# Performance work log

Measured on AMD Instinct MI355X. Metric: run time of the kernel, lower is better.

Reference implementation:

```python
import jax, jax.numpy as jnp
import numpy as np

DIM = 1024
HEADS = 16
HEAD_DIM = DIM // HEADS
SCALE = HEAD_DIM ** -0.5
EPS = 1e-5


def _ln(x, g, b):
    m = jnp.mean(x, axis=-1, keepdims=True)
    v = jnp.mean((x - m) ** 2, axis=-1, keepdims=True)
    return (x - m) * jax.lax.rsqrt(v + EPS) * g + b


def setup_inputs() -> dict:
    key = jax.random.key(0)
    ks = jax.random.split(key, 12)
    B, N, C = 4, 1024, DIM
    s = lambda fan: 1.0 / np.sqrt(fan)
    return {
        "src_q": jax.random.normal(ks[0], (B, N, C), jnp.float32),
        "src_kv": jax.random.normal(ks[1], (B, N, C), jnp.float32),
        "gq": jnp.ones((C,), jnp.float32), "bq": jnp.zeros((C,), jnp.float32),
        "gkv": jnp.ones((C,), jnp.float32), "bkv": jnp.zeros((C,), jnp.float32),
        "Wq": jax.random.normal(ks[2], (C, C), jnp.float32) * s(C),
        "Wkv": jax.random.normal(ks[3], (C, 2 * C), jnp.float32) * s(C),
        "Wproj": jax.random.normal(ks[4], (C, C), jnp.float32) * s(C),
        "bproj": jnp.zeros((C,), jnp.float32),
        "gn": jnp.ones((C,), jnp.float32), "bn": jnp.zeros((C,), jnp.float32),
        "W1": jax.random.normal(ks[5], (C, 4 * C), jnp.float32) * s(C),
        "b1": jnp.zeros((4 * C,), jnp.float32),
        "W2": jax.random.normal(ks[6], (4 * C, C), jnp.float32) * s(4 * C),
        "b2": jnp.zeros((C,), jnp.float32),
    }


def reference(src_q, src_kv, gq, bq, gkv, bkv, Wq, Wkv, Wproj, bproj,
              gn, bn, W1, b1, W2, b2):
    B, N, C = src_q.shape
    qn = _ln(src_q, gq, bq)
    kvn = _ln(src_kv, gkv, bkv)
    # Q: [B, H, N, d]
    Q = (qn @ Wq).reshape(B, N, HEADS, HEAD_DIM).transpose(0, 2, 1, 3)
    KV = (kvn @ Wkv).reshape(B, N, 2, HEADS, HEAD_DIM).transpose(2, 0, 3, 1, 4)
    K, V = KV[0], KV[1]
    attn = jnp.einsum('bhqd,bhkd->bhqk', Q, K) * SCALE
    attn = jax.nn.softmax(attn, axis=-1)
    # NOTE: original code multiplies by scale a second time here (faithful)
    x = jnp.einsum('bhqk,bhkd->bhqd', attn, V) * SCALE
    x = x.transpose(0, 2, 1, 3).reshape(B, N, C)
    x = x @ Wproj + bproj
    src = src_q + x               # residual (drop_path = identity in eval)
    src = _ln(src, gn, bn)
    h = jax.nn.gelu(src @ W1 + b1, approximate=False)
    src2 = h @ W2 + b2
    return src + src2
```

## Files before the change

### kernel.cpp

```cpp
#include <hip/hip_runtime.h>
#include <hip/hip_bf16.h>
#include <math.h>

typedef __bf16 bf16;
typedef __bf16 bf16x2 __attribute__((ext_vector_type(2)));
typedef __bf16 bf16x8 __attribute__((ext_vector_type(8)));
typedef float f32x4 __attribute__((ext_vector_type(4)));
typedef float f32x16 __attribute__((ext_vector_type(16)));
typedef unsigned int u32;
typedef unsigned int u32x2 __attribute__((ext_vector_type(2)));
typedef unsigned int u32x4 __attribute__((ext_vector_type(4)));

#define SCALE 0.125f

#define GLOAD_LDS16(gptr, lptr)                                      \
  __builtin_amdgcn_global_load_lds(                                  \
      (const __attribute__((address_space(1))) void*)(gptr),         \
      (__attribute__((address_space(3))) void*)(lptr), 16, 0, 0)

template <int N>
__device__ __forceinline__ void vmcnt_wait() {
  if constexpr (N == 0) asm volatile("s_waitcnt vmcnt(0)" ::: "memory");
  else if constexpr (N == 4) asm volatile("s_waitcnt vmcnt(4)" ::: "memory");
  else if constexpr (N == 6) asm volatile("s_waitcnt vmcnt(6)" ::: "memory");
  else static_assert(N == 0 || N == 4 || N == 6, "unsupported vmcnt");
}

__device__ __forceinline__ void xcd_swz(int gx, int gy, int& x, int& y) {
  int w = blockIdx.x + gx * blockIdx.y;
  int nwg = gx * gy;
  int wp = (w & 7) * (nwg >> 3) + (w >> 3);
  int xi = wp & 7;
  int t = wp >> 3;
  y = t % gy;
  x = (t / gy) * 8 + xi;
}

__device__ __forceinline__ u32 pk_bf16(float lo, float hi) {
  bf16x2 t;
  t[0] = (bf16)lo;
  t[1] = (bf16)hi;
  return __builtin_bit_cast(u32, t);
}

__device__ __forceinline__ void plane32_swap(u32& a, u32& b) {
  asm volatile("v_permlane32_swap_b32 %0, %1" : "+v"(a), "+v"(b));
}

__global__ __launch_bounds__(256) void ln_f32(const float* __restrict__ x,
                                              const float* __restrict__ g,
                                              const float* __restrict__ b,
                                              bf16* __restrict__ y) {
  long base = (long)blockIdx.x * 1024;
  int tid = threadIdx.x;
  float v[4];
#pragma unroll
  for (int i = 0; i < 4; i++) v[i] = x[base + tid + i * 256];
  float s1 = v[0] + v[1] + v[2] + v[3];
  float s2 = v[0] * v[0] + v[1] * v[1] + v[2] * v[2] + v[3] * v[3];
#pragma unroll
  for (int off = 32; off; off >>= 1) {
    s1 += __shfl_xor(s1, off);
    s2 += __shfl_xor(s2, off);
  }
  __shared__ float aux[2][4];
  int wave = tid >> 6, lane = tid & 63;
  if (lane == 0) { aux[0][wave] = s1; aux[1][wave] = s2; }
  __syncthreads();
  float S1 = aux[0][0] + aux[0][1] + aux[0][2] + aux[0][3];
  float S2 = aux[1][0] + aux[1][1] + aux[1][2] + aux[1][3];
  float mean = S1 * (1.0f / 1024.0f);
  float var = S2 * (1.0f / 1024.0f) - mean * mean;
  float rs = rsqrtf(var + 1e-5f);
#pragma unroll
  for (int i = 0; i < 4; i++) {
    int c = tid + i * 256;
    y[base + c] = (bf16)(((v[i] - mean) * rs) * g[c] + b[c]);
  }
}

__global__ __launch_bounds__(256) void transpose_w(const float* __restrict__ W,
                                                   bf16* __restrict__ Wt,
                                                   int K, int N) {
  __shared__ bf16 tile[64][66];
  int n0 = blockIdx.x * 64, k0 = blockIdx.y * 64;
  int c = threadIdx.x & 63, r4 = threadIdx.x >> 6;
#pragma unroll
  for (int i = 0; i < 16; i++)
    tile[i * 4 + r4][c] = (bf16)W[(long)(k0 + i * 4 + r4) * N + n0 + c];
  __syncthreads();
#pragma unroll
  for (int i = 0; i < 16; i++)
    Wt[(long)(n0 + i * 4 + r4) * K + k0 + c] = tile[c][i * 4 + r4];
}

__global__ __launch_bounds__(256) void extract_vt(const bf16* __restrict__ KV,
                                                  bf16* __restrict__ Vt) {
  __shared__ bf16 tile[64][66];
  int bh = blockIdx.z, b = bh >> 4, h = bh & 15;
  const bf16* src = KV + (long)b * 1024 * 2048 + 1024 + h * 64;
  bf16* dst = Vt + (long)bh * 64 * 1024;
  int n0 = blockIdx.x * 64;
  int c = threadIdx.x & 63, r4 = threadIdx.x >> 6;
#pragma unroll
  for (int i = 0; i < 16; i++)
    tile[i * 4 + r4][c] = src[(long)(n0 + i * 4 + r4) * 2048 + c];
  __syncthreads();
#pragma unroll
  for (int i = 0; i < 16; i++)
    dst[(long)(i * 4 + r4) * 1024 + n0 + c] = tile[c][i * 4 + r4];
}

__global__ __launch_bounds__(256) void attn_fused(
    const bf16* __restrict__ Q,
    const bf16* __restrict__ KV,
    const bf16* __restrict__ Vt,
    bf16* __restrict__ X) {
  __shared__ __align__(16) bf16 Qs[128 * 64];
  __shared__ __align__(16) bf16 Ks[2][64 * 128];
  __shared__ __align__(16) bf16 Vs[2][64 * 128];
  int tid = threadIdx.x, wave = tid >> 6, lane = tid & 63;
  int l31 = lane & 31, h = lane >> 5;
  int bqx, bhy;
  xcd_swz(8, 64, bqx, bhy);
  int bh = bhy, b = bh >> 4, hd = bh & 15;
  const bf16* Qb = Q + (long)b * 1048576 + hd * 64;
  const bf16* Kb = KV + (long)b * 2097152 + hd * 64;
  const bf16* Vb = Vt + (long)bh * 65536;
  bf16* Xb = X + (long)b * 1048576 + hd * 64;
  int q0 = bqx * 128;

  const bf16* gk[4];
  const bf16* gv[4];
  int eoKV[4];
#pragma unroll
  for (int t = 0; t < 4; t++) {
    int eo = (t * 256 + tid) * 8;
    eoKV[t] = eo;
    int r2 = eo >> 7, pp = (eo & 127) >> 3, q = pp ^ (r2 & 15);
    gk[t] = &Kb[(long)(r2 + ((q >> 3) << 6)) * 2048 + ((q & 7) << 3)];
    gv[t] = &Vb[(long)r2 * 1024 + (q << 3)];
  }

#pragma unroll
  for (int t = 0; t < 4; t++) {
    int eo = (t * 256 + tid) * 8;
    int r = eo >> 6, p = (eo & 63) >> 3;
    int c = (p ^ (r & 7)) << 3;
    GLOAD_LDS16(&Qb[(long)(q0 + r) * 1024 + c], &Qs[eo]);
  }
#pragma unroll
  for (int t = 0; t < 4; t++) GLOAD_LDS16(gk[t], &Ks[0][eoKV[t]]);
#pragma unroll
  for (int t = 0; t < 4; t++) GLOAD_LDS16(gv[t], &Vs[0][eoKV[t]]);
  __syncthreads();

  bf16x8 qf[4];
  {
    int r = wave * 32 + l31;
#pragma unroll
    for (int dw = 0; dw < 4; dw++) {
      int p = (dw * 2 + h) ^ (r & 7);
      qf[dw] = *(const bf16x8*)&Qs[r * 64 + p * 8];
    }
  }

  const float C = 0.18033688011112042f;
  float m_run = -1e30f, l_run = 0.0f;
  f32x16 acc[2] = {};
  int cur = 0;

  for (int kc = 0; kc < 8; kc++) {
    if (kc < 7) {
#pragma unroll
      for (int t = 0; t < 4; t++)
        GLOAD_LDS16(gk[t] + (long)(kc + 1) * 128 * 2048, &Ks[cur ^ 1][eoKV[t]]);
#pragma unroll
      for (int t = 0; t < 4; t++)
        GLOAD_LDS16(gv[t] + (kc + 1) * 128, &Vs[cur ^ 1][eoKV[t]]);
    }
    const bf16* ks = Ks[cur];
    const bf16* vs = Vs[cur];

    f32x16 s[4] = {};
#pragma unroll
    for (int kt = 0; kt < 4; kt++) {
      int k = kt * 32 + l31;
      int r2 = k & 63, hi = k >> 6;
#pragma unroll
      for (int dw = 0; dw < 4; dw++) {
        int p = (hi * 8 + dw * 2 + h) ^ (r2 & 15);
        bf16x8 kf = *(const bf16x8*)&ks[r2 * 128 + p * 8];
        s[kt] = __builtin_amdgcn_mfma_f32_32x32x16_bf16(kf, qf[dw], s[kt], 0, 0, 0);
      }
    }

    float mk[4];
#pragma unroll
    for (int kt = 0; kt < 4; kt++) {
      float m01 = fmaxf(fmaxf(s[kt][0], s[kt][1]), fmaxf(s[kt][2], s[kt][3]));
      float m23 = fmaxf(fmaxf(s[kt][4], s[kt][5]), fmaxf(s[kt][6], s[kt][7]));
      float m45 = fmaxf(fmaxf(s[kt][8], s[kt][9]), fmaxf(s[kt][10], s[kt][11]));
      float m67 = fmaxf(fmaxf(s[kt][12], s[kt][13]), fmaxf(s[kt][14], s[kt][15]));
      mk[kt] = fmaxf(fmaxf(m01, m23), fmaxf(m45, m67));
    }
    float mx = fmaxf(fmaxf(mk[0], mk[1]), fmaxf(mk[2], mk[3]));
    mx = fmaxf(mx, __shfl_xor(mx, 32));
    float m_new = fmaxf(m_run, mx);
    float alpha = exp2f((m_run - m_new) * C);
    m_run = m_new;
    float mc = m_new * C;
    float rk[4];
#pragma unroll
    for (int kt = 0; kt < 4; kt++) {
      float r0 = 0.0f;
#pragma unroll
      for (int r = 0; r < 16; r++) {
        float pv = exp2f(s[kt][r] * C - mc);
        s[kt][r] = pv;
        r0 += pv;
      }
      rk[kt] = r0;
    }
    float rs = (rk[0] + rk[1]) + (rk[2] + rk[3]);
    rs += __shfl_xor(rs, 32);
    l_run = l_run * alpha + rs;
#pragma unroll
    for (int nt = 0; nt < 2; nt++)
#pragma unroll
      for (int r = 0; r < 16; r++) acc[nt][r] *= alpha;

#pragma unroll
    for (int kw = 0; kw < 8; kw++) {
      int kt = kw >> 1, rb = (kw & 1) * 8;
      u32 wA = pk_bf16(s[kt][rb + 0], s[kt][rb + 1]);
      u32 wB = pk_bf16(s[kt][rb + 2], s[kt][rb + 3]);
      u32 wC = pk_bf16(s[kt][rb + 4], s[kt][rb + 5]);
      u32 wD = pk_bf16(s[kt][rb + 6], s[kt][rb + 7]);
      plane32_swap(wA, wC);
      plane32_swap(wB, wD);
      u32x4 wv = {wA, wB, wC, wD};
      bf16x8 pf = __builtin_bit_cast(bf16x8, wv);
#pragma unroll
      for (int nt = 0; nt < 2; nt++) {
        int r2 = nt * 32 + l31;
        int p = (kw * 2 + h) ^ (r2 & 15);
        bf16x8 vf = *(const bf16x8*)&vs[r2 * 128 + p * 8];
        acc[nt] = __builtin_amdgcn_mfma_f32_32x32x16_bf16(vf, pf, acc[nt], 0, 0, 0);
      }
    }

    if (kc < 7) {
      __syncthreads();
      cur ^= 1;
    }
  }

  float fs = SCALE / l_run;
  bf16* Os = Qs;
  int qrow = wave * 32 + l31;
#pragma unroll
  for (int nt = 0; nt < 2; nt++)
#pragma unroll
    for (int g = 0; g < 4; g++) {
      u32 w0 = pk_bf16(acc[nt][g * 4 + 0] * fs, acc[nt][g * 4 + 1] * fs);
      u32 w1 = pk_bf16(acc[nt][g * 4 + 2] * fs, acc[nt][g * 4 + 3] * fs);
      int s8 = nt * 8 + g * 2 + h;
      int phys = s8 ^ (qrow & 15);
      u32x2 wv = {w0, w1};
      *(u32x2*)&Os[qrow * 64 + phys * 4] = wv;
    }
  int rrow = wave * 32 + (lane >> 1);
  int cbase = (lane & 1) * 32;
#pragma unroll
  for (int t2 = 0; t2 < 4; t2++) {
    int s0 = (lane & 1) * 8 + t2 * 2;
    u32x2 a = *(u32x2*)&Os[rrow * 64 + ((s0 ^ (rrow & 15)) * 4)];
    u32x2 bb = *(u32x2*)&Os[rrow * 64 + (((s0 + 1) ^ (rrow & 15)) * 4)];
    u32x4 o4 = {a[0], a[1], bb[0], bb[1]};
    *(u32x4*)&Xb[(long)(q0 + rrow) * 1024 + cbase + t2 * 8] = o4;
  }
}

template <int BM, int BN, int WR, int WC, int EPI, int CF32, int RBF16>
__global__ __launch_bounds__(512) void gemm_p(
    const bf16* __restrict__ A, int lda,
    const bf16* __restrict__ B, int ldb,
    void* __restrict__ Cv, int ldc, int K,
    const float* __restrict__ bias,
    const void* __restrict__ resv, int ldr) {
  constexpr int MT = BM / (16 * WR);
  constexpr int NT = BN / (16 * WC);
  constexpr int L = (BM + BN) / 64;
  constexpr int LA = BM / 64;
  constexpr int AE = BM * 64;
  constexpr int BUFE = (BM + BN) * 64;
  __shared__ __align__(16) bf16 lds[3 * BUFE];
  int tid = threadIdx.x;
  int wave = tid >> 6, lane = tid & 63;
  int wm = wave / WC, wn = wave % WC;
  int quad = lane >> 4, l16 = lane & 15;
  int bx, by;
  xcd_swz(gridDim.x, gridDim.y, bx, by);
  int m0 = by * BM, n0 = bx * BN;

  const bf16* gp[L];
  int lo[L];
#pragma unroll
  for (int i = 0; i < L; i++) {
    if (i < LA) {
      int eo = (i * 512 + tid) * 8;
      int r = eo >> 6, p = (eo & 63) >> 3;
      int c = (p ^ (r & 7)) << 3;
      gp[i] = &A[(long)(m0 + r) * lda + c];
      lo[i] = eo;
    } else {
      int eo = ((i - LA) * 512 + tid) * 8;
      int r = eo >> 6, p = (eo & 63) >> 3;
      int c = (p ^ (r & 7)) << 3;
      gp[i] = &B[(long)(n0 + r) * ldb + c];
      lo[i] = AE + eo;
    }
  }

  int ntk = K >> 6;
#pragma unroll
  for (int i = 0; i < L; i++) GLOAD_LDS16(gp[i], &lds[lo[i]]);
#pragma unroll
  for (int i = 0; i < L; i++) gp[i] += 64;
#pragma unroll
  for (int i = 0; i < L; i++) GLOAD_LDS16(gp[i], &lds[BUFE + lo[i]]);
#pragma unroll
  for (int i = 0; i < L; i++) gp[i] += 64;
  vmcnt_wait<L>();
  asm volatile("" ::: "memory");
  __builtin_amdgcn_s_barrier();

  f32x4 acc[MT][NT] = {};
  int b = 0;
  for (int t = 0; t < ntk; t++) {
    const bf16* Al = &lds[b * BUFE];
    const bf16* Bl = &lds[b * BUFE + AE];
    int b2 = b + 2; if (b2 >= 3) b2 -= 3;
    bool more = (t + 2) < ntk;

    bf16x8 af[2][MT], bv[2][NT];
#pragma unroll
    for (int ks = 0; ks < 2; ks++) {
#pragma unroll
      for (int mt = 0; mt < MT; mt++) {
        int row = wm * (BM / WR) + mt * 16 + l16;
        int p = (ks * 4 + quad) ^ (row & 7);
        af[ks][mt] = *(const bf16x8*)&Al[row * 64 + p * 8];
      }
#pragma unroll
      for (int nt = 0; nt < NT; nt++) {
        int row = wn * (BN / WC) + nt * 16 + l16;
        int p = (ks * 4 + quad) ^ (row & 7);
        bv[ks][nt] = *(const bf16x8*)&Bl[row * 64 + p * 8];
      }
    }
    if (more) {
#pragma unroll
      for (int i = 0; i < L; i++) GLOAD_LDS16(gp[i], &lds[b2 * BUFE + lo[i]]);
    }
    asm volatile("s_waitcnt lgkmcnt(0)" ::: "memory");
    __builtin_amdgcn_sched_barrier(0);
    __builtin_amdgcn_s_setprio(1);
#pragma unroll
    for (int ks = 0; ks < 2; ks++)
#pragma unroll
      for (int mt = 0; mt < MT; mt++)
#pragma unroll
        for (int nt = 0; nt < NT; nt++)
          acc[mt][nt] = __builtin_amdgcn_mfma_f32_16x16x32_bf16(
              af[ks][mt], bv[ks][nt], acc[mt][nt], 0, 0, 0);
    __builtin_amdgcn_s_setprio(0);
    __builtin_amdgcn_sched_barrier(0);
    if (more) {
      vmcnt_wait<L>();
    } else if (t + 1 < ntk) {
      vmcnt_wait<0>();
    }
    if (t + 1 < ntk) {
      asm volatile("" ::: "memory");
      __builtin_amdgcn_s_barrier();
    }
#pragma unroll
    for (int i = 0; i < L; i++) gp[i] += 64;
    b += 1; if (b == 3) b = 0;
  }

  int gm = m0 + wm * (BM / WR), gn = n0 + wn * (BN / WC);
#pragma unroll
  for (int nt = 0; nt < NT; nt++) {
    int col = gn + nt * 16 + l16;
    float bvb = (EPI != 0) ? bias[col] : 0.0f;
#pragma unroll
    for (int mt = 0; mt < MT; mt++) {
#pragma unroll
      for (int r = 0; r < 4; r++) {
        int row = gm + mt * 16 + quad * 4 + r;
        float v = acc[mt][nt][r] + bvb;
        if (EPI == 2) {
          v = 0.5f * v * (1.0f + erff(v * 0.70710678118654752f));
        } else if (EPI == 1) {
          float rv = RBF16 ? (float)((const bf16*)resv)[(long)row * ldr + col]
                           : ((const float*)resv)[(long)row * ldr + col];
          v += rv;
        }
        if (CF32)
          ((float*)Cv)[(long)row * ldc + col] = v;
        else
          ((bf16*)Cv)[(long)row * ldc + col] = (bf16)v;
      }
    }
  }
}

template <int EPI, int CF32, int RBF16>
__global__ __launch_bounds__(512) void gemm_256(
    const bf16* __restrict__ A, int lda,
    const bf16* __restrict__ B, int ldb,
    void* __restrict__ Cv, int ldc, int K,
    const float* __restrict__ bias,
    const void* __restrict__ resv, int ldr) {
  constexpr int AE = 256 * 64;
  constexpr int BUFE = 512 * 64;
  __shared__ __align__(16) bf16 lds[2 * BUFE];
  int tid = threadIdx.x;
  int wave = tid >> 6, lane = tid & 63;
  int wm = wave >> 2, wn = wave & 3;
  int quad = lane >> 4, l16 = lane & 15;
  int bx, by;
  xcd_swz(gridDim.x, gridDim.y, bx, by);
  int m0 = by * 256, n0 = bx * 256;

  const bf16* gp[8];
  int lo[8];
#pragma unroll
  for (int i = 0; i < 8; i++) {
    if (i < 4) {
      int eo = (i * 512 + tid) * 8;
      int r = eo >> 6, p = (eo & 63) >> 3;
      int c = (p ^ (r & 7)) << 3;
      gp[i] = &A[(long)(m0 + r) * lda + c];
      lo[i] = eo;
    } else {
      int eo = ((i - 4) * 512 + tid) * 8;
      int r = eo >> 6, p = (eo & 63) >> 3;
      int c = (p ^ (r & 7)) << 3;
      gp[i] = &B[(long)(n0 + r) * ldb + c];
      lo[i] = AE + eo;
    }
  }

  int ntk = K >> 6;
#pragma unroll
  for (int i = 0; i < 8; i++) GLOAD_LDS16(gp[i], &lds[lo[i]]);
#pragma unroll
  for (int i = 0; i < 8; i++) gp[i] += 64;
  vmcnt_wait<0>();
  asm volatile("" ::: "memory");
  __builtin_amdgcn_s_barrier();

  f32x4 acc[8][4] = {};
  for (int t = 0; t < ntk; t++) {
    const bf16* Al = &lds[(t & 1) * BUFE];
    const bf16* Bl = &lds[(t & 1) * BUFE + AE];
    if (t + 1 < ntk) {
#pragma unroll
      for (int i = 0; i < 8; i++)
        GLOAD_LDS16(gp[i], &lds[((t + 1) & 1) * BUFE + lo[i]]);
#pragma unroll
      for (int i = 0; i < 8; i++) gp[i] += 64;
    }
#pragma unroll
    for (int ks = 0; ks < 2; ks++) {
      bf16x8 af[8], bv[4];
#pragma unroll
      for (int mi = 0; mi < 8; mi++) {
        int row = wm * 128 + mi * 16 + l16;
        int p = (ks * 4 + quad) ^ (row & 7);
        af[mi] = *(const bf16x8*)&Al[row * 64 + p * 8];
      }
#pragma unroll
      for (int ni = 0; ni < 4; ni++) {
        int row = wn * 64 + ni * 16 + l16;
        int p = (ks * 4 + quad) ^ (row & 7);
        bv[ni] = *(const bf16x8*)&Bl[row * 64 + p * 8];
      }
      asm volatile("s_waitcnt lgkmcnt(0)" ::: "memory");
      __builtin_amdgcn_sched_barrier(0);
      __builtin_amdgcn_s_setprio(1);
#pragma unroll
      for (int mi = 0; mi < 8; mi++)
#pragma unroll
        for (int ni = 0; ni < 4; ni++)
          acc[mi][ni] = __builtin_amdgcn_mfma_f32_16x16x32_bf16(
              af[mi], bv[ni], acc[mi][ni], 0, 0, 0);
      __builtin_amdgcn_s_setprio(0);
      __builtin_amdgcn_sched_barrier(0);
    }
    if (t + 1 < ntk) {
      vmcnt_wait<0>();
      asm volatile("" ::: "memory");
      __builtin_amdgcn_s_barrier();
    }
  }

  int gm = m0 + wm * 128, gn = n0 + wn * 64;
#pragma unroll
  for (int ni = 0; ni < 4; ni++) {
    int col = gn + ni * 16 + l16;
    float bvb = (EPI != 0) ? bias[col] : 0.0f;
#pragma unroll
    for (int mi = 0; mi < 8; mi++) {
#pragma unroll
      for (int r = 0; r < 4; r++) {
        int row = gm + mi * 16 + quad * 4 + r;
        float v = acc[mi][ni][r] + bvb;
        if (EPI == 2) {
          v = 0.5f * v * (1.0f + erff(v * 0.70710678118654752f));
        } else if (EPI == 1) {
          float rv = RBF16 ? (float)((const bf16*)resv)[(long)row * ldr + col]
                           : ((const float*)resv)[(long)row * ldr + col];
          v += rv;
        }
        if (CF32)
          ((float*)Cv)[(long)row * ldc + col] = v;
        else
          ((bf16*)Cv)[(long)row * ldc + col] = (bf16)v;
      }
    }
  }
}

extern "C" void kernel_launch(void* const* d_in, const int* in_sizes, int n_in,
                              void* d_out, int out_size, void* d_ws, size_t ws_size,
                              hipStream_t stream) {
  const float* src_q  = (const float*)d_in[0];
  const float* src_kv = (const float*)d_in[1];
  const float* gq     = (const float*)d_in[2];
  const float* bq     = (const float*)d_in[3];
  const float* gkv    = (const float*)d_in[4];
  const float* bkv    = (const float*)d_in[5];
  const float* Wq     = (const float*)d_in[6];
  const float* Wkv    = (const float*)d_in[7];
  const float* Wproj  = (const float*)d_in[8];
  const float* bproj  = (const float*)d_in[9];
  const float* gn     = (const float*)d_in[10];
  const float* bn     = (const float*)d_in[11];
  const float* W1     = (const float*)d_in[12];
  const float* b1     = (const float*)d_in[13];
  const float* W2     = (const float*)d_in[14];
  const float* b2     = (const float*)d_in[15];
  float* out = (float*)d_out;

  char* ws = (char*)d_ws;
  const long MB = 1024 * 1024;
  bf16* Wq_t    = (bf16*)(ws + 0 * MB);
  bf16* Wkv_t   = (bf16*)(ws + 2 * MB);
  bf16* Wproj_t = (bf16*)(ws + 6 * MB);
  bf16* W1_t    = (bf16*)(ws + 8 * MB);
  bf16* W2_t    = (bf16*)(ws + 16 * MB);
  bf16* qn      = (bf16*)(ws + 24 * MB);
  bf16* kvn     = (bf16*)(ws + 32 * MB);
  bf16* Qm      = (bf16*)(ws + 40 * MB);
  bf16* KVm     = (bf16*)(ws + 48 * MB);
  bf16* Vt      = (bf16*)(ws + 64 * MB);
  bf16* xbuf    = (bf16*)(ws + 24 * MB);
  float* tbuf   = (float*)(ws + 48 * MB);
  bf16* sbuf    = (bf16*)(ws + 64 * MB);
  bf16* hbuf    = (bf16*)(ws + 72 * MB);

  transpose_w<<<dim3(16, 16), 256, 0, stream>>>(Wq, Wq_t, 1024, 1024);
  transpose_w<<<dim3(32, 16), 256, 0, stream>>>(Wkv, Wkv_t, 1024, 2048);
  transpose_w<<<dim3(16, 16), 256, 0, stream>>>(Wproj, Wproj_t, 1024, 1024);
  transpose_w<<<dim3(64, 16), 256, 0, stream>>>(W1, W1_t, 1024, 4096);
  transpose_w<<<dim3(16, 64), 256, 0, stream>>>(W2, W2_t, 4096, 1024);

  ln_f32<<<4096, 256, 0, stream>>>(src_q, gq, bq, qn);
  ln_f32<<<4096, 256, 0, stream>>>(src_kv, gkv, bkv, kvn);

  gemm_p<128, 128, 2, 4, 0, 0, 0><<<dim3(8, 32), 512, 0, stream>>>(
      qn, 1024, Wq_t, 1024, Qm, 1024, 1024, nullptr, nullptr, 0);
  gemm_p<256, 128, 4, 2, 0, 0, 0><<<dim3(16, 16), 512, 0, stream>>>(
      kvn, 1024, Wkv_t, 1024, KVm, 2048, 1024, nullptr, nullptr, 0);
  extract_vt<<<dim3(16, 1, 64), 256, 0, stream>>>(KVm, Vt);

  attn_fused<<<dim3(8, 64), 256, 0, stream>>>(Qm, KVm, Vt, xbuf);

  gemm_p<128, 128, 2, 4, 1, 1, 0><<<dim3(8, 32), 512, 0, stream>>>(
      xbuf, 1024, Wproj_t, 1024, tbuf, 1024, 1024, bproj, src_q, 1024);
  ln_f32<<<4096, 256, 0, stream>>>(tbuf, gn, bn, sbuf);
  gemm_256<2, 0, 0><<<dim3(16, 16), 512, 0, stream>>>(
      sbuf, 1024, W1_t, 1024, hbuf, 4096, 1024, b1, nullptr, 0);
  gemm_p<128, 128, 2, 4, 1, 1, 1><<<dim3(8, 32), 512, 0, stream>>>(
      hbuf, 4096, W2_t, 4096, out, 1024, 4096, b2, sbuf, 1024);
}
```

Baseline: 366.2 us.

## Restructure W1 GEMM into eight-phase pipelined schedule with half-K staged loads

Rewrites the 256x256 FC1 GEMM kernel so each 64-wide K tile is split into two 32-wide halves stored separately in LDS with a new XOR swizzle. Global-to-LDS copies are issued one half-tile at a time, interleaved between four MFMA phases separated by barriers, and a vmcnt(6) wait replaces the full drain. The aim is to overlap memory traffic with MFMA work and hide LDS read latency. It also adds a launch bound of two blocks per CU, which caps registers per thread and may cause spills. The extra barriers add synchronisation cost.

```diff
diff --git a/kernel.cpp b/kernel.cpp
--- a/kernel.cpp
+++ b/kernel.cpp
@@ -419,15 +419,13 @@
 }
 
 template <int EPI, int CF32, int RBF16>
-__global__ __launch_bounds__(512) void gemm_256(
+__global__ __launch_bounds__(512, 2) void gemm_8p(
     const bf16* __restrict__ A, int lda,
     const bf16* __restrict__ B, int ldb,
     void* __restrict__ Cv, int ldc, int K,
     const float* __restrict__ bias,
     const void* __restrict__ resv, int ldr) {
-  constexpr int AE = 256 * 64;
-  constexpr int BUFE = 512 * 64;
-  __shared__ __align__(16) bf16 lds[2 * BUFE];
+  __shared__ __align__(16) bf16 lds[65536];
   int tid = threadIdx.x;
   int wave = tid >> 6, lane = tid & 63;
   int wm = wave >> 2, wn = wave & 3;
@@ -436,78 +434,141 @@
   xcd_swz(gridDim.x, gridDim.y, bx, by);
   int m0 = by * 256, n0 = bx * 256;
 
-  const bf16* gp[8];
-  int lo[8];
-#pragma unroll
-  for (int i = 0; i < 8; i++) {
-    if (i < 4) {
-      int eo = (i * 512 + tid) * 8;
-      int r = eo >> 6, p = (eo & 63) >> 3;
-      int c = (p ^ (r & 7)) << 3;
-      gp[i] = &A[(long)(m0 + r) * lda + c];
-      lo[i] = eo;
-    } else {
-      int eo = ((i - 4) * 512 + tid) * 8;
-      int r = eo >> 6, p = (eo & 63) >> 3;
-      int c = (p ^ (r & 7)) << 3;
-      gp[i] = &B[(long)(n0 + r) * ldb + c];
-      lo[i] = AE + eo;
-    }
-  }
-
+  int eo0 = tid * 8, eo1 = 4096 + tid * 8;
+  const bf16 *sA0, *sA1, *sB0, *sB1;
+  {
+    int r0 = eo0 >> 5, p0 = (eo0 >> 3) & 3, q0 = p0 ^ ((r0 >> 1) & 3);
+    int r1 = eo1 >> 5, p1 = (eo1 >> 3) & 3, q1 = p1 ^ ((r1 >> 1) & 3);
+    sA0 = &A[(long)(m0 + r0) * lda + q0 * 8];
+    sA1 = &A[(long)(m0 + r1) * lda + q1 * 8];
+    sB0 = &B[(long)(n0 + r0) * ldb + q0 * 8];
+    sB1 = &B[(long)(n0 + r1) * ldb + q1 * 8];
+  }
   int ntk = K >> 6;
-#pragma unroll
-  for (int i = 0; i < 8; i++) GLOAD_LDS16(gp[i], &lds[lo[i]]);
-#pragma unroll
-  for (int i = 0; i < 8; i++) gp[i] += 64;
-  vmcnt_wait<0>();
+
+#define STAGE_HALF(ts, j)                                                     \
+  {                                                                           \
+    long ko = (long)(ts) * 64 + ((j) & 1) * 32;                               \
+    int bas = (((ts) & 1) << 15) + (((j) >> 1) << 14) + (((j) & 1) << 13);    \
+    if ((j) >> 1) {                                                           \
+      GLOAD_LDS16(sB0 + ko, &lds[bas + eo0]);                                 \
+      GLOAD_LDS16(sB1 + ko, &lds[bas + eo1]);                                 \
+    } else {                                                                  \
+      GLOAD_LDS16(sA0 + ko, &lds[bas + eo0]);                                 \
+      GLOAD_LDS16(sA1 + ko, &lds[bas + eo1]);                                 \
+    }                                                                         \
+  }
+
+  STAGE_HALF(0, 0) STAGE_HALF(0, 1) STAGE_HALF(0, 2) STAGE_HALF(0, 3)
+  STAGE_HALF(1, 0) STAGE_HALF(1, 1) STAGE_HALF(1, 2)
+  vmcnt_wait<6>();
   asm volatile("" ::: "memory");
   __builtin_amdgcn_s_barrier();
 
   f32x4 acc[8][4] = {};
+  int rA = wm * 128 + l16;
+  int rB = wn * 64 + l16;
+
   for (int t = 0; t < ntk; t++) {
-    const bf16* Al = &lds[(t & 1) * BUFE];
-    const bf16* Bl = &lds[(t & 1) * BUFE + AE];
-    if (t + 1 < ntk) {
-#pragma unroll
-      for (int i = 0; i < 8; i++)
-        GLOAD_LDS16(gp[i], &lds[((t + 1) & 1) * BUFE + lo[i]]);
-#pragma unroll
-      for (int i = 0; i < 8; i++) gp[i] += 64;
-    }
-#pragma unroll
-    for (int ks = 0; ks < 2; ks++) {
-      bf16x8 af[8], bv[4];
-#pragma unroll
-      for (int mi = 0; mi < 8; mi++) {
-        int row = wm * 128 + mi * 16 + l16;
-        int p = (ks * 4 + quad) ^ (row & 7);
-        af[mi] = *(const bf16x8*)&Al[row * 64 + p * 8];
-      }
-#pragma unroll
-      for (int ni = 0; ni < 4; ni++) {
-        int row = wn * 64 + ni * 16 + l16;
-        int p = (ks * 4 + quad) ^ (row & 7);
-        bv[ni] = *(const bf16x8*)&Bl[row * 64 + p * 8];
-      }
-      asm volatile("s_waitcnt lgkmcnt(0)" ::: "memory");
-      __builtin_amdgcn_sched_barrier(0);
-      __builtin_amdgcn_s_setprio(1);
-#pragma unroll
-      for (int mi = 0; mi < 8; mi++)
-#pragma unroll
-        for (int ni = 0; ni < 4; ni++)
-          acc[mi][ni] = __builtin_amdgcn_mfma_f32_16x16x32_bf16(
-              af[mi], bv[ni], acc[mi][ni], 0, 0, 0);
-      __builtin_amdgcn_s_setprio(0);
-      __builtin_amdgcn_sched_barrier(0);
-    }
-    if (t + 1 < ntk) {
-      vmcnt_wait<0>();
-      asm volatile("" ::: "memory");
-      __builtin_amdgcn_s_barrier();
-    }
-  }
+    const bf16* Ld = &lds[(t & 1) << 15];
+    bf16x8 af[8], af2[8], b0, b1, b2, b3;
+
+#pragma unroll
+    for (int mi = 0; mi < 8; mi++) {
+      int r = rA + mi * 16;
+      af[mi] = *(const bf16x8*)&Ld[r * 32 + (quad ^ ((r >> 1) & 3)) * 8];
+    }
+    {
+      int r = rB;
+      b0 = *(const bf16x8*)&Ld[16384 + r * 32 + (quad ^ ((r >> 1) & 3)) * 8];
+      r = rB + 16;
+      b1 = *(const bf16x8*)&Ld[16384 + r * 32 + (quad ^ ((r >> 1) & 3)) * 8];
+    }
+    if (t + 1 < ntk) STAGE_HALF(t + 1, 3)
+    asm volatile("" ::: "memory");
+    __builtin_amdgcn_s_barrier();
+    asm volatile("s_waitcnt lgkmcnt(0)" ::: "memory");
+    __builtin_amdgcn_s_setprio(1);
+#pragma unroll
+    for (int mi = 0; mi < 8; mi++)
+      acc[mi][0] = __builtin_amdgcn_mfma_f32_16x16x32_bf16(af[mi], b0, acc[mi][0], 0, 0, 0);
+#pragma unroll
+    for (int mi = 0; mi < 8; mi++)
+      acc[mi][1] = __builtin_amdgcn_mfma_f32_16x16x32_bf16(af[mi], b1, acc[mi][1], 0, 0, 0);
+    __builtin_amdgcn_s_setprio(0);
+    asm volatile("" ::: "memory");
+    __builtin_amdgcn_s_barrier();
+
+    {
+      int r = rB + 32;
+      b2 = *(const bf16x8*)&Ld[16384 + r * 32 + (quad ^ ((r >> 1) & 3)) * 8];
+      r = rB + 48;
+      b3 = *(const bf16x8*)&Ld[16384 + r * 32 + (quad ^ ((r >> 1) & 3)) * 8];
+    }
+#pragma unroll
+    for (int mi = 0; mi < 8; mi++) {
+      int r = rA + mi * 16;
+      af2[mi] = *(const bf16x8*)&Ld[8192 + r * 32 + (quad ^ ((r >> 1) & 3)) * 8];
+    }
+    if (t + 2 < ntk) STAGE_HALF(t + 2, 0)
+    asm volatile("" ::: "memory");
+    __builtin_amdgcn_s_barrier();
+    asm volatile("s_waitcnt lgkmcnt(0)" ::: "memory");
+    __builtin_amdgcn_s_setprio(1);
+#pragma unroll
+    for (int mi = 0; mi < 8; mi++)
+      acc[mi][2] = __builtin_amdgcn_mfma_f32_16x16x32_bf16(af[mi], b2, acc[mi][2], 0, 0, 0);
+#pragma unroll
+    for (int mi = 0; mi < 8; mi++)
+      acc[mi][3] = __builtin_amdgcn_mfma_f32_16x16x32_bf16(af[mi], b3, acc[mi][3], 0, 0, 0);
+    __builtin_amdgcn_s_setprio(0);
+    asm volatile("" ::: "memory");
+    __builtin_amdgcn_s_barrier();
+
+    {
+      int r = rB;
+      b0 = *(const bf16x8*)&Ld[24576 + r * 32 + (quad ^ ((r >> 1) & 3)) * 8];
+      r = rB + 16;
+      b1 = *(const bf16x8*)&Ld[24576 + r * 32 + (quad ^ ((r >> 1) & 3)) * 8];
+    }
+    if (t + 2 < ntk) STAGE_HALF(t + 2, 1)
+    asm volatile("" ::: "memory");
+    __builtin_amdgcn_s_barrier();
+    asm volatile("s_waitcnt lgkmcnt(0)" ::: "memory");
+    __builtin_amdgcn_s_setprio(1);
+#pragma unroll
+    for (int mi = 0; mi < 8; mi++)
+      acc[mi][0] = __builtin_amdgcn_mfma_f32_16x16x32_bf16(af2[mi], b0, acc[mi][0], 0, 0, 0);
+#pragma unroll
+    for (int mi = 0; mi < 8; mi++)
+      acc[mi][1] = __builtin_amdgcn_mfma_f32_16x16x32_bf16(af2[mi], b1, acc[mi][1], 0, 0, 0);
+    __builtin_amdgcn_s_setprio(0);
+    asm volatile("" ::: "memory");
+    __builtin_amdgcn_s_barrier();
+
+    {
+      int r = rB + 32;
+      b2 = *(const bf16x8*)&Ld[24576 + r * 32 + (quad ^ ((r >> 1) & 3)) * 8];
+      r = rB + 48;
+      b3 = *(const bf16x8*)&Ld[24576 + r * 32 + (quad ^ ((r >> 1) & 3)) * 8];
+    }
+    if (t + 2 < ntk) STAGE_HALF(t + 2, 2)
+    vmcnt_wait<6>();
+    asm volatile("" ::: "memory");
+    __builtin_amdgcn_s_barrier();
+    asm volatile("s_waitcnt lgkmcnt(0)" ::: "memory");
+    __builtin_amdgcn_s_setprio(1);
+#pragma unroll
+    for (int mi = 0; mi < 8; mi++)
+      acc[mi][2] = __builtin_amdgcn_mfma_f32_16x16x32_bf16(af2[mi], b2, acc[mi][2], 0, 0, 0);
+#pragma unroll
+    for (int mi = 0; mi < 8; mi++)
+      acc[mi][3] = __builtin_amdgcn_mfma_f32_16x16x32_bf16(af2[mi], b3, acc[mi][3], 0, 0, 0);
+    __builtin_amdgcn_s_setprio(0);
+    asm volatile("" ::: "memory");
+    __builtin_amdgcn_s_barrier();
+  }
+#undef STAGE_HALF
 
   int gm = m0 + wm * 128, gn = n0 + wn * 64;
 #pragma unroll
@@ -594,7 +655,7 @@
   gemm_p<128, 128, 2, 4, 1, 1, 0><<<dim3(8, 32), 512, 0, stream>>>(
       xbuf, 1024, Wproj_t, 1024, tbuf, 1024, 1024, bproj, src_q, 1024);
   ln_f32<<<4096, 256, 0, stream>>>(tbuf, gn, bn, sbuf);
-  gemm_256<2, 0, 0><<<dim3(16, 16), 512, 0, stream>>>(
+  gemm_8p<2, 0, 0><<<dim3(16, 16), 512, 0, stream>>>(
       sbuf, 1024, W1_t, 1024, hbuf, 4096, 1024, b1, nullptr, 0);
   gemm_p<128, 128, 2, 4, 1, 1, 1><<<dim3(8, 32), 512, 0, stream>>>(
       hbuf, 4096, W2_t, 4096, out, 1024, 4096, b2, sbuf, 1024);
```

New measurement: 367.3 us. No clear change (+0.3%).
